# Kernel optimization log

Hardware: AMD Instinct MI355X
Metric: run time of the kernel (lower is better)

Reference implementation:

```python
import jax, jax.numpy as jnp
import numpy as np

L, H, NH, FF = 12, 768, 12, 3072
HD = H // NH
B, T = 8, 512
SCALE = 1.0 / float(np.sqrt(HD))
EPS = 1e-12


def setup_inputs() -> dict:
    key = jax.random.key(0)
    ks = jax.random.split(key, 10)
    s = jnp.float32(0.02)

    def p(k, shape):
        return jax.random.normal(k, shape, dtype=jnp.float32) * s

    return {
        "hidden_states": jax.random.normal(ks[0], (B, T, H), dtype=jnp.float32),
        "attention_mask": jnp.ones((B, T), dtype=jnp.float32),
        "Wq": p(ks[1], (L, H, H)), "bq": jnp.zeros((L, H), jnp.float32),
        "Wk": p(ks[2], (L, H, H)), "bk": jnp.zeros((L, H), jnp.float32),
        "Wv": p(ks[3], (L, H, H)), "bv": jnp.zeros((L, H), jnp.float32),
        "Wao": p(ks[4], (L, H, H)), "bao": jnp.zeros((L, H), jnp.float32),
        "ln1_g": jnp.ones((L, H), jnp.float32), "ln1_b": jnp.zeros((L, H), jnp.float32),
        "Wi": p(ks[5], (L, H, FF)), "bi": jnp.zeros((L, FF), jnp.float32),
        "Wo": p(ks[6], (L, FF, H)), "bo": jnp.zeros((L, H), jnp.float32),
        "ln2_g": jnp.ones((L, H), jnp.float32), "ln2_b": jnp.zeros((L, H), jnp.float32),
    }


def _layernorm(x, g, b):
    m = jnp.mean(x, axis=-1, keepdims=True)
    v = jnp.mean((x - m) ** 2, axis=-1, keepdims=True)
    return (x - m) * jax.lax.rsqrt(v + EPS) * g + b


def _encoder(hidden_states, attention_mask, params):
    # additive mask: (1 - mask) * -10000, broadcast to [B, 1, 1, T]
    add_mask = (1.0 - attention_mask)[:, None, None, :] * -10000.0

    def layer(x, p):
        wq, bq, wk, bk, wv, bv, wao, bao, g1, b1, wi, bi, wo, bo, g2, b2 = p
        q = (x @ wq + bq).reshape(B, T, NH, HD)
        k = (x @ wk + bk).reshape(B, T, NH, HD)
        v = (x @ wv + bv).reshape(B, T, NH, HD)
        scores = jnp.einsum('bihd,bjhd->bhij', q, k) * SCALE + add_mask
        probs = jax.nn.softmax(scores, axis=-1)  # dropout p=0 (eval)
        ctx = jnp.einsum('bhij,bjhd->bihd', probs, v).reshape(B, T, H)
        attn_out = _layernorm(ctx @ wao + bao + x, g1, b1)
        ff = jax.nn.gelu(attn_out @ wi + bi, approximate=False)
        out = _layernorm(ff @ wo + bo + attn_out, g2, b2)
        return out, None

    out, _ = jax.lax.scan(layer, hidden_states, params)
    return out


def reference(hidden_states, attention_mask, Wq, bq, Wk, bk, Wv, bv, Wao, bao,
              ln1_g, ln1_b, Wi, bi, Wo, bo, ln2_g, ln2_b):
    params = (Wq, bq, Wk, bk, Wv, bv, Wao, bao, ln1_g, ln1_b, Wi, bi, Wo, bo, ln2_g, ln2_b)
    return _encoder(hidden_states, attention_mask, params)
```

## Files before the change

### kernel.cpp

```cpp
#include <hip/hip_runtime.h>
#include <hip/hip_bf16.h>

typedef __bf16 bf16;
typedef __attribute__((ext_vector_type(8))) __bf16 bf16x8;
typedef __attribute__((ext_vector_type(4))) float f32x4;

#define MFMA16(a, b, c) __builtin_amdgcn_mfma_f32_16x16x32_bf16((a), (b), (c), 0, 0, 0)

#define SYNC_VM(N) do { asm volatile("s_waitcnt vmcnt(" #N ")" ::: "memory"); \
    __builtin_amdgcn_s_barrier(); __builtin_amdgcn_sched_barrier(0); } while (0)
#define SYNC_LGKM() do { asm volatile("s_waitcnt lgkmcnt(0)" ::: "memory"); \
    __builtin_amdgcn_s_barrier(); __builtin_amdgcn_sched_barrier(0); } while (0)

__device__ __forceinline__ void async16(const bf16* g, bf16* l) {
    __builtin_amdgcn_global_load_lds((__attribute__((address_space(1))) void*)(g),
                                     (__attribute__((address_space(3))) void*)(l), 16, 0, 0);
}

__device__ __forceinline__ void xcd_swizzle(int& bx, int& by, int& bz) {
    const int gx = gridDim.x, gy = gridDim.y;
    const int nwg = gx * gy * gridDim.z;
    const int lin = blockIdx.x + gx * (blockIdx.y + gy * blockIdx.z);
    const int xcd = lin & 7, seq = lin >> 3;
    const int q = nwg >> 3, r = nwg & 7;
    const int nl = (xcd < r ? xcd * (q + 1) : r * (q + 1) + (xcd - r) * q) + seq;
    bx = nl % gx;
    const int t = nl / gx;
    by = t % gy;
    bz = t / gy;
}

template <int MODE, int BM>
__global__ __launch_bounds__(256) void gemm_kernel(
    const bf16* __restrict__ A, const bf16* __restrict__ WT,
    const float* __restrict__ b0, const float* __restrict__ b1, const float* __restrict__ b2,
    int s1, int s2,
    void* __restrict__ o0, void* __restrict__ o1,
    int N, int K, int Kpart)
{
    constexpr int MT = BM / 32;
    __shared__ __align__(16) bf16 sA[2][BM * 32];
    __shared__ __align__(16) bf16 sB[2][128 * 32];

    const int tid  = threadIdx.x;
    const int lane = tid & 63;
    const int wave = tid >> 6;
    const int quad = lane >> 4;
    const int l15  = lane & 15;
    const int wm   = (wave >> 1) * (BM / 2);
    const int wn   = (wave & 1) * 64;

    int bxs, bys, bzs;
    xcd_swizzle(bxs, bys, bzs);
    const int bm = bys * BM;
    const int bn = bxs * 128;
    const int kbase = bzs * Kpart;

    f32x4 acc[MT][4];
#pragma unroll
    for (int i = 0; i < MT; i++)
#pragma unroll
        for (int j = 0; j < 4; j++)
#pragma unroll
            for (int r = 0; r < 4; r++) acc[i][j][r] = 0.0f;

    const int idx1 = tid + 256;
    const int ra0 = tid >> 2,  ca0 = (((tid  & 3) ^ ((ra0 >> 1) & 3)) * 8);
    const int rb1 = idx1 >> 2, cb1 = (((idx1 & 3) ^ ((rb1 >> 1) & 3)) * 8);

    const bf16* Arow0 = A + (size_t)(bm + ra0) * K + kbase + ca0;
    const bf16* Arow1 = (BM == 128) ? A + (size_t)(bm + rb1) * K + kbase + cb1 : A;
    const bf16* Brow0 = WT + (size_t)(bn + ra0) * K + kbase + ca0;
    const bf16* Brow1 = WT + (size_t)(bn + rb1) * K + kbase + cb1;

    const int nk = Kpart >> 5;

    async16(Arow0, sA[0] + tid * 8);
    if (BM == 128) async16(Arow1, sA[0] + idx1 * 8);
    async16(Brow0, sB[0] + tid * 8);
    async16(Brow1, sB[0] + idx1 * 8);

    const int chF = (quad ^ ((l15 >> 1) & 3)) * 8;

    int cur = 0;
    for (int kt = 0; kt < nk; kt++) {
        if (kt + 1 < nk) {
            const int ko = (kt + 1) * 32;
            async16(Arow0 + ko, sA[cur ^ 1] + tid * 8);
            if (BM == 128) async16(Arow1 + ko, sA[cur ^ 1] + idx1 * 8);
            async16(Brow0 + ko, sB[cur ^ 1] + tid * 8);
            async16(Brow1 + ko, sB[cur ^ 1] + idx1 * 8);
            if (BM == 128) SYNC_VM(4);
            else           SYNC_VM(3);
        } else {
            SYNC_VM(0);
        }
        bf16x8 af[MT], bfr[4];
#pragma unroll
        for (int i = 0; i < MT; i++)
            af[i] = *(const bf16x8*)(sA[cur] + (wm + i * 16 + l15) * 32 + chF);
#pragma unroll
        for (int i = 0; i < 4; i++)
            bfr[i] = *(const bf16x8*)(sB[cur] + (wn + i * 16 + l15) * 32 + chF);
#pragma unroll
        for (int mt = 0; mt < MT; mt++)
#pragma unroll
            for (int nt = 0; nt < 4; nt++)
                acc[mt][nt] = MFMA16(af[mt], bfr[nt], acc[mt][nt]);
        SYNC_LGKM();
        cur ^= 1;
    }

    void* outp = (bzs == 0) ? o0 : o1;

#pragma unroll
    for (int nt = 0; nt < 4; nt++) {
        const int col = bn + wn + nt * 16 + l15;
        float bias = 0.0f;
        if (MODE != 1)
            bias = (col < s1) ? b0[col] : (col < s2) ? b1[col - s1] : b2[col - s2];
#pragma unroll
        for (int mt = 0; mt < MT; mt++) {
#pragma unroll
            for (int r = 0; r < 4; r++) {
                const int row = bm + wm + mt * 16 + quad * 4 + r;
                float v = acc[mt][nt][r] + bias;
                if (MODE == 2) v = 0.5f * v * (1.0f + erff(v * 0.70710678118654752f));
                if (MODE == 1) ((float*)outp)[(size_t)row * N + col] = v;
                else           ((bf16*)outp)[(size_t)row * N + col] = (bf16)v;
            }
        }
    }
}

__global__ __launch_bounds__(256) void vtrans_kernel(
    const bf16* __restrict__ qkv, bf16* __restrict__ vT)
{
    const int bh = blockIdx.y;
    const int b = bh / 12, h = bh - b * 12;
    const int k0 = blockIdx.x * 128;
    __shared__ __align__(16) bf16 tile[128 * 72];
    const int tid = threadIdx.x;
    const bf16* src = qkv + (size_t)(b * 512 + k0) * 2304 + 1536 + h * 64;
#pragma unroll
    for (int i = 0; i < 4; i++) {
        const int idx = i * 256 + tid;
        const int r = idx >> 3, c = (idx & 7) * 8;
        *(uint4*)(tile + r * 72 + c) = *(const uint4*)(src + (size_t)r * 2304 + c);
    }
    __syncthreads();
    bf16* dst = vT + (size_t)bh * 64 * 512 + k0;
#pragma unroll
    for (int i = 0; i < 4; i++) {
        const int idx = i * 256 + tid;
        const int d = idx & 63, kg = idx >> 6;
        alignas(16) bf16 tmp[8];
#pragma unroll
        for (int e = 0; e < 8; e++) tmp[e] = tile[(kg * 8 + e) * 72 + d];
        *(uint4*)(dst + (size_t)d * 512 + kg * 8) = *(uint4*)tmp;
    }
}

__global__ __launch_bounds__(256) void attn_kernel(
    const bf16* __restrict__ qkv, const bf16* __restrict__ vT,
    const float* __restrict__ mask, bf16* __restrict__ ctx)
{
    int bxs, bys, bzs;
    xcd_swizzle(bxs, bys, bzs);
    const int b = bzs, h = bys, q0 = bxs * 32;
    const int bh = b * 12 + h;
    const int tid = threadIdx.x, lane = tid & 63, wave = tid >> 6;
    const int quad = lane >> 4, l15 = lane & 15;
    const int mt = wave & 1;
    const int whi = wave >> 1;

    __shared__ __align__(16) bf16 sKV[2][64 * 64];
    __shared__ __align__(16) bf16 sS[32 * 520];
    __shared__ float sAM[512];
    __shared__ float sRed[256];
    __shared__ float sRow[32];

    for (int i = tid; i < 512; i += 256)
        sAM[i] = (1.0f - mask[b * 512 + i]) * -10000.0f;

    const size_t RS = 2304;
    const bf16* Qrow = qkv + (size_t)(b * 512 + q0 + mt * 16 + l15) * RS + h * 64;
    const bf16x8 aQ0 = *(const bf16x8*)(Qrow + quad * 8);
    const bf16x8 aQ1 = *(const bf16x8*)(Qrow + 32 + quad * 8);

    const int c0 = tid, c1 = tid + 256;
    const int r0 = c0 >> 3, r1 = c1 >> 3;
    const int sc0 = ((c0 & 7) ^ (r0 & 7)) * 8;
    const int sc1 = ((c1 & 7) ^ (r1 & 7)) * 8;

    const bf16* Kbase = qkv + (size_t)(b * 512) * RS + 768 + h * 64;

    async16(Kbase + (size_t)(r0) * RS + sc0, (bf16*)sKV[0] + c0 * 8);
    async16(Kbase + (size_t)(r1) * RS + sc1, (bf16*)sKV[0] + c1 * 8);

#pragma unroll
    for (int kt = 0; kt < 8; kt++) {
        const int cur = kt & 1;
        if (kt < 7) {
            async16(Kbase + (size_t)((kt + 1) * 64 + r0) * RS + sc0, (bf16*)sKV[cur ^ 1] + c0 * 8);
            async16(Kbase + (size_t)((kt + 1) * 64 + r1) * RS + sc1, (bf16*)sKV[cur ^ 1] + c1 * 8);
            SYNC_VM(2);
        } else {
            SYNC_VM(0);
        }
#pragma unroll
        for (int n = 0; n < 2; n++) {
            const int nt = whi * 2 + n;
            const int krow = nt * 16 + l15;
            const int sw = krow & 7;
            bf16x8 bK0 = *(const bf16x8*)(sKV[cur] + krow * 64 + ((quad ^ sw) * 8));
            bf16x8 bK1 = *(const bf16x8*)(sKV[cur] + krow * 64 + (((4 + quad) ^ sw) * 8));
            f32x4 accS;
#pragma unroll
            for (int r = 0; r < 4; r++) accS[r] = 0.0f;
            accS = MFMA16(aQ0, bK0, accS);
            accS = MFMA16(aQ1, bK1, accS);
#pragma unroll
            for (int r = 0; r < 4; r++) {
                const int row = mt * 16 + quad * 4 + r;
                sS[row * 520 + kt * 64 + nt * 16 + l15] = (bf16)accS[r];
            }
        }
        SYNC_LGKM();
    }

    const bf16* Vbase = vT + (size_t)bh * 64 * 512;
    async16(Vbase + (size_t)r0 * 512 + sc0, (bf16*)sKV[0] + c0 * 8);
    async16(Vbase + (size_t)r1 * 512 + sc1, (bf16*)sKV[0] + c1 * 8);

    {
        const int r = tid >> 3, p = tid & 7;
        float mx = -1e30f;
#pragma unroll
        for (int t = 0; t < 8; t++) {
            const int v0 = (p + 8 * t) * 8;
            bf16x8 pv = *(const bf16x8*)(sS + r * 520 + v0);
#pragma unroll
            for (int e = 0; e < 8; e++)
                mx = fmaxf(mx, (float)pv[e] * 0.125f + sAM[v0 + e]);
        }
        sRed[r * 8 + p] = mx;
        SYNC_LGKM();
#pragma unroll
        for (int q = 0; q < 8; q++) mx = fmaxf(mx, sRed[r * 8 + q]);
        float sum = 0.0f;
#pragma unroll
        for (int t = 0; t < 8; t++) {
            const int v0 = (p + 8 * t) * 8;
            bf16x8 pv = *(const bf16x8*)(sS + r * 520 + v0);
            bf16x8 ev;
#pragma unroll
            for (int e = 0; e < 8; e++) {
                const float x = __expf((float)pv[e] * 0.125f + sAM[v0 + e] - mx);
                sum += x;
                ev[e] = (bf16)x;
            }
            *(bf16x8*)(sS + r * 520 + v0) = ev;
        }
        SYNC_LGKM();
        sRed[r * 8 + p] = sum;
        SYNC_LGKM();
        if (p == 0) {
            float s = 0.0f;
#pragma unroll
            for (int q = 0; q < 8; q++) s += sRed[r * 8 + q];
            sRow[r] = s;
        }
    }

    f32x4 accO[2];
#pragma unroll
    for (int i = 0; i < 2; i++)
#pragma unroll
        for (int r = 0; r < 4; r++) accO[i][r] = 0.0f;

#pragma unroll
    for (int kt = 0; kt < 8; kt++) {
        const int cur = kt & 1;
        if (kt < 7) {
            async16(Vbase + (size_t)r0 * 512 + (kt + 1) * 64 + sc0, (bf16*)sKV[cur ^ 1] + c0 * 8);
            async16(Vbase + (size_t)r1 * 512 + (kt + 1) * 64 + sc1, (bf16*)sKV[cur ^ 1] + c1 * 8);
            SYNC_VM(2);
        } else {
            SYNC_VM(0);
        }
#pragma unroll
        for (int kk = 0; kk < 2; kk++) {
            bf16x8 aP = *(const bf16x8*)(sS + (mt * 16 + l15) * 520 + kt * 64 + kk * 32 + quad * 8);
#pragma unroll
            for (int n = 0; n < 2; n++) {
                const int vrow = whi * 32 + n * 16 + l15;
                bf16x8 bV = *(const bf16x8*)(sKV[cur] + vrow * 64 + (((kk * 4 + quad) ^ (vrow & 7)) * 8));
                accO[n] = MFMA16(aP, bV, accO[n]);
            }
        }
        SYNC_LGKM();
    }
#pragma unroll
    for (int n = 0; n < 2; n++) {
#pragma unroll
        for (int r = 0; r < 4; r++) {
            const int row = mt * 16 + quad * 4 + r;
            const float o = accO[n][r] / sRow[row];
            ctx[(size_t)(b * 512 + q0 + row) * 768 + h * 64 + whi * 32 + n * 16 + l15] = (bf16)o;
        }
    }
}

template <int NP>
__global__ __launch_bounds__(256) void ln_kernel(
    const float* __restrict__ p0, const float* __restrict__ p1,
    const float* __restrict__ bias, const float* __restrict__ resid,
    const float* __restrict__ g, const float* __restrict__ bb,
    bf16* __restrict__ out_bf, float* __restrict__ out_f32)
{
    const int row = blockIdx.x;
    const int tid = threadIdx.x;
    __shared__ float sS[4], sQ[4];

    float x[3], s = 0.0f, sq = 0.0f;
#pragma unroll
    for (int j = 0; j < 3; j++) {
        const int c = tid + j * 256;
        const size_t idx = (size_t)row * 768 + c;
        float v = p0[idx] + bias[c] + resid[idx];
        if (NP > 1) v += p1[idx];
        x[j] = v; s += v; sq += v * v;
    }
#pragma unroll
    for (int off = 32; off; off >>= 1) { s += __shfl_down(s, off); sq += __shfl_down(sq, off); }
    if ((tid & 63) == 0) { sS[tid >> 6] = s; sQ[tid >> 6] = sq; }
    __syncthreads();
    s  = sS[0] + sS[1] + sS[2] + sS[3];
    sq = sQ[0] + sQ[1] + sQ[2] + sQ[3];
    const float mean = s * (1.0f / 768.0f);
    float var = sq * (1.0f / 768.0f) - mean * mean;
    var = fmaxf(var, 0.0f);
    const float rstd = rsqrtf(var + 1e-12f);
#pragma unroll
    for (int j = 0; j < 3; j++) {
        const int c = tid + j * 256;
        const float v = (x[j] - mean) * rstd * g[c] + bb[c];
        out_bf[(size_t)row * 768 + c] = (bf16)v;
        out_f32[(size_t)row * 768 + c] = v;
    }
}

__global__ __launch_bounds__(256) void transpose_kernel(
    const float* __restrict__ Wq, const float* __restrict__ Wk, const float* __restrict__ Wv,
    const float* __restrict__ Wao, const float* __restrict__ Wi, const float* __restrict__ Wo,
    bf16* __restrict__ wT)
{
    __shared__ bf16 tile[64 * 68];
    int id = blockIdx.x;
    const float* src; bf16* dst; int Kd, Nd;
    if (id < 576) {
        const int w = id / 144; id -= w * 144;
        Kd = 768; Nd = 768;
        src = (w == 0) ? Wq : (w == 1) ? Wk : (w == 2) ? Wv : Wao;
        dst = wT + (size_t)w * 589824;
    } else if (id < 1152) {
        id -= 576; Kd = 768; Nd = 3072; src = Wi; dst = wT + 2359296;
    } else {
        id -= 1152; Kd = 3072; Nd = 768; src = Wo; dst = wT + 4718592;
    }
    const int tn = Nd >> 6;
    const int tr = id / tn, tc = id - tr * tn;
    const int r0 = tr * 64, c0 = tc * 64;
    const int tid = threadIdx.x;

#pragma unroll
    for (int i = 0; i < 4; i++) {
        const int idx = i * 256 + tid;
        const int r = idx >> 4, c4 = (idx & 15) * 4;
        const float4 f = *(const float4*)(src + (size_t)(r0 + r) * Nd + c0 + c4);
        alignas(8) bf16 q[4] = {(bf16)f.x, (bf16)f.y, (bf16)f.z, (bf16)f.w};
        *(ushort4*)(tile + r * 68 + c4) = *(ushort4*)q;
    }
    __syncthreads();
#pragma unroll
    for (int i = 0; i < 4; i++) {
        const int idx = i * 256 + tid;
        const int n = idx >> 4, kc = (idx & 15) * 4;
        alignas(8) bf16 tmp[4];
#pragma unroll
        for (int e = 0; e < 4; e++) tmp[e] = tile[(kc + e) * 68 + n];
        *(ushort4*)(dst + (size_t)(c0 + n) * Kd + r0 + kc) = *(ushort4*)tmp;
    }
}

__global__ __launch_bounds__(256) void convert_kernel(
    const float* __restrict__ in, bf16* __restrict__ out, int n)
{
    const int i = blockIdx.x * 256 + threadIdx.x;
    if (i < n) out[i] = (bf16)in[i];
}

extern "C" void kernel_launch(void* const* d_in, const int* in_sizes, int n_in,
                              void* d_out, int out_size, void* d_ws, size_t ws_size,
                              hipStream_t stream)
{
    const float* hidden = (const float*)d_in[0];
    const float* mask   = (const float*)d_in[1];
    const float* Wq  = (const float*)d_in[2];  const float* bq  = (const float*)d_in[3];
    const float* Wk  = (const float*)d_in[4];  const float* bk  = (const float*)d_in[5];
    const float* Wv  = (const float*)d_in[6];  const float* bv  = (const float*)d_in[7];
    const float* Wao = (const float*)d_in[8];  const float* bao = (const float*)d_in[9];
    const float* g1  = (const float*)d_in[10]; const float* be1 = (const float*)d_in[11];
    const float* Wi  = (const float*)d_in[12]; const float* bi  = (const float*)d_in[13];
    const float* Wo  = (const float*)d_in[14]; const float* bo  = (const float*)d_in[15];
    const float* g2  = (const float*)d_in[16]; const float* be2 = (const float*)d_in[17];

    char* ws = (char*)d_ws;
    bf16*  wT    = (bf16*)(ws);
    bf16*  qkv   = (bf16*)(ws + 14155776);
    bf16*  vT    = (bf16*)(ws + 33030144);
    bf16*  ctx   = (bf16*)(ws + 39321600);
    bf16*  attnb = (bf16*)(ws + 45613056);
    bf16*  xb    = (bf16*)(ws + 51904512);
    float* xf    = (float*)(ws + 58195968);
    float* attnf = (float*)(ws + 70778880);
    bf16*  ffh   = (bf16*)(ws + 14155776);
    float* pA0   = (float*)(ws + 14155776);
    float* pF0   = (float*)(ws + 39321600);
    float* pF1   = (float*)(ws + 83361792);

    convert_kernel<<<12288, 256, 0, stream>>>(hidden, xb, 3145728);

    for (int l = 0; l < 12; l++) {
        transpose_kernel<<<1728, 256, 0, stream>>>(
            Wq + (size_t)l * 589824, Wk + (size_t)l * 589824, Wv + (size_t)l * 589824,
            Wao + (size_t)l * 589824, Wi + (size_t)l * 2359296, Wo + (size_t)l * 2359296, wT);

        gemm_kernel<0, 64><<<dim3(18, 64, 1), 256, 0, stream>>>(
            xb, wT, bq + l * 768, bk + l * 768, bv + l * 768, 768, 1536,
            qkv, nullptr, 2304, 768, 768);

        vtrans_kernel<<<dim3(4, 96), 256, 0, stream>>>(qkv, vT);

        attn_kernel<<<dim3(16, 12, 8), 256, 0, stream>>>(qkv, vT, mask, ctx);

        gemm_kernel<1, 64><<<dim3(6, 64, 1), 256, 0, stream>>>(
            ctx, wT + 1769472, nullptr, nullptr, nullptr, 0, 0,
            pA0, nullptr, 768, 768, 768);

        const float* resid1 = (l == 0) ? hidden : xf;
        ln_kernel<1><<<4096, 256, 0, stream>>>(
            pA0, nullptr, bao + l * 768, resid1, g1 + l * 768, be1 + l * 768, attnb, attnf);

        gemm_kernel<2, 128><<<dim3(24, 32, 1), 256, 0, stream>>>(
            attnb, wT + 2359296, bi + l * 3072, bi + l * 3072, bi + l * 3072, 3072, 3072,
            ffh, nullptr, 3072, 768, 768);

        gemm_kernel<1, 64><<<dim3(6, 64, 2), 256, 0, stream>>>(
            ffh, wT + 4718592, nullptr, nullptr, nullptr, 0, 0,
            pF0, pF1, 768, 3072, 1536);

        float* f32dst = (l == 11) ? (float*)d_out : xf;
        ln_kernel<2><<<4096, 256, 0, stream>>>(
            pF0, pF1, bo + l * 768, attnf, g2 + l * 768, be2 + l * 768, xb, f32dst);
    }
}
```

Before: 2.462 ms.

## Add single-wave 64x64 GEMM kernel and 3-way split-K for projections

```diff
diff --git a/kernel.cpp b/kernel.cpp
--- a/kernel.cpp
+++ b/kernel.cpp
@@ -28,6 +28,103 @@
     const int t = nl / gx;
     by = t % gy;
     bz = t / gy;
+}
+
+template <int MODE>
+__global__ __launch_bounds__(64) void gemm1w_kernel(
+    const bf16* __restrict__ A, const bf16* __restrict__ WT,
+    const float* __restrict__ b0, const float* __restrict__ b1, const float* __restrict__ b2,
+    int s1, int s2,
+    float* __restrict__ o0, float* __restrict__ o1, float* __restrict__ o2,
+    bf16* __restrict__ ob,
+    int N, int K, int Kpart)
+{
+    __shared__ __align__(16) bf16 sA[2][64 * 32];
+    __shared__ __align__(16) bf16 sB[2][64 * 32];
+
+    const int l    = threadIdx.x;
+    const int quad = l >> 4;
+    const int l15  = l & 15;
+
+    int bxs, bys, bzs;
+    xcd_swizzle(bxs, bys, bzs);
+    const int bm = bys * 64;
+    const int bn = bxs * 64;
+    const int kbase = bzs * Kpart;
+
+    int rS[4], cS[4];
+#pragma unroll
+    for (int g = 0; g < 4; g++) {
+        rS[g] = g * 16 + (l >> 2);
+        cS[g] = (((l & 3) ^ ((rS[g] >> 1) & 3)) * 8);
+    }
+    const bf16* Abase = A  + kbase;
+    const bf16* Bbase = WT + kbase;
+
+    const int nk = Kpart >> 5;
+
+    auto stage = [&](int kt, int buf) {
+#pragma unroll
+        for (int g = 0; g < 4; g++)
+            async16(Abase + (size_t)(bm + rS[g]) * K + kt * 32 + cS[g], sA[buf] + (g * 64 + l) * 8);
+#pragma unroll
+        for (int g = 0; g < 4; g++)
+            async16(Bbase + (size_t)(bn + rS[g]) * K + kt * 32 + cS[g], sB[buf] + (g * 64 + l) * 8);
+    };
+
+    f32x4 acc[4][4];
+#pragma unroll
+    for (int i = 0; i < 4; i++)
+#pragma unroll
+        for (int j = 0; j < 4; j++)
+#pragma unroll
+            for (int r = 0; r < 4; r++) acc[i][j][r] = 0.0f;
+
+    stage(0, 0);
+    if (nk > 1) stage(1, 1);
+
+    const int chF = (quad ^ ((l15 >> 1) & 3)) * 8;
+
+    for (int kt = 0; kt < nk; kt++) {
+        const int cur = kt & 1;
+        if (kt + 1 < nk) { asm volatile("s_waitcnt vmcnt(8)" ::: "memory"); }
+        else             { asm volatile("s_waitcnt vmcnt(0)" ::: "memory"); }
+        __builtin_amdgcn_sched_barrier(0);
+        bf16x8 af[4], bfr[4];
+#pragma unroll
+        for (int i = 0; i < 4; i++)
+            af[i] = *(const bf16x8*)(sA[cur] + (i * 16 + l15) * 32 + chF);
+#pragma unroll
+        for (int i = 0; i < 4; i++)
+            bfr[i] = *(const bf16x8*)(sB[cur] + (i * 16 + l15) * 32 + chF);
+#pragma unroll
+        for (int mt = 0; mt < 4; mt++)
+#pragma unroll
+            for (int nt = 0; nt < 4; nt++)
+                acc[mt][nt] = MFMA16(af[mt], bfr[nt], acc[mt][nt]);
+        __builtin_amdgcn_sched_barrier(0);
+        if (kt + 2 < nk) stage(kt + 2, cur);
+    }
+
+    float* po = (bzs == 0) ? o0 : (bzs == 1) ? o1 : o2;
+
+#pragma unroll
+    for (int nt = 0; nt < 4; nt++) {
+        const int col = bn + nt * 16 + l15;
+        float bias = 0.0f;
+        if (MODE == 0)
+            bias = (col < s1) ? b0[col] : (col < s2) ? b1[col - s1] : b2[col - s2];
+#pragma unroll
+        for (int mt = 0; mt < 4; mt++) {
+#pragma unroll
+            for (int r = 0; r < 4; r++) {
+                const int row = bm + mt * 16 + quad * 4 + r;
+                const float v = acc[mt][nt][r] + bias;
+                if (MODE == 1) po[(size_t)row * N + col] = v;
+                else           ob[(size_t)row * N + col] = (bf16)v;
+            }
+        }
+    }
 }
 
 template <int MODE, int BM>
@@ -314,10 +411,10 @@
 
 template <int NP>
 __global__ __launch_bounds__(256) void ln_kernel(
-    const float* __restrict__ p0, const float* __restrict__ p1,
-    const float* __restrict__ bias, const float* __restrict__ resid,
-    const float* __restrict__ g, const float* __restrict__ bb,
-    bf16* __restrict__ out_bf, float* __restrict__ out_f32)
+    const float* p0, const float* p1, const float* p2,
+    const float* bias, const float* resid,
+    const float* g, const float* bb,
+    bf16* out_bf, float* out_f32)
 {
     const int row = blockIdx.x;
     const int tid = threadIdx.x;
@@ -330,6 +427,7 @@
         const size_t idx = (size_t)row * 768 + c;
         float v = p0[idx] + bias[c] + resid[idx];
         if (NP > 1) v += p1[idx];
+        if (NP > 2) v += p2[idx];
         x[j] = v; s += v; sq += v * v;
     }
 #pragma unroll
@@ -427,8 +525,11 @@
     float* attnf = (float*)(ws + 70778880);
     bf16*  ffh   = (bf16*)(ws + 14155776);
     float* pA0   = (float*)(ws + 14155776);
+    float* pA1   = (float*)(ws + 26738688);
+    float* pA2   = (float*)(ws + 83361792);
     float* pF0   = (float*)(ws + 39321600);
-    float* pF1   = (float*)(ws + 83361792);
+    float* pF1   = (float*)(ws + 58195968);
+    float* pF2   = (float*)(ws + 83361792);
 
     convert_kernel<<<12288, 256, 0, stream>>>(hidden, xb, 3145728);
 
@@ -437,32 +538,32 @@
             Wq + (size_t)l * 589824, Wk + (size_t)l * 589824, Wv + (size_t)l * 589824,
             Wao + (size_t)l * 589824, Wi + (size_t)l * 2359296, Wo + (size_t)l * 2359296, wT);
 
-        gemm_kernel<0, 64><<<dim3(18, 64, 1), 256, 0, stream>>>(
+        gemm1w_kernel<0><<<dim3(36, 64, 1), 64, 0, stream>>>(
             xb, wT, bq + l * 768, bk + l * 768, bv + l * 768, 768, 1536,
-            qkv, nullptr, 2304, 768, 768);
+            nullptr, nullptr, nullptr, qkv, 2304, 768, 768);
 
         vtrans_kernel<<<dim3(4, 96), 256, 0, stream>>>(qkv, vT);
 
         attn_kernel<<<dim3(16, 12, 8), 256, 0, stream>>>(qkv, vT, mask, ctx);
 
-        gemm_kernel<1, 64><<<dim3(6, 64, 1), 256, 0, stream>>>(
+        gemm1w_kernel<1><<<dim3(12, 64, 3), 64, 0, stream>>>(
             ctx, wT + 1769472, nullptr, nullptr, nullptr, 0, 0,
-            pA0, nullptr, 768, 768, 768);
+            pA0, pA1, pA2, nullptr, 768, 768, 256);
 
         const float* resid1 = (l == 0) ? hidden : xf;
-        ln_kernel<1><<<4096, 256, 0, stream>>>(
-            pA0, nullptr, bao + l * 768, resid1, g1 + l * 768, be1 + l * 768, attnb, attnf);
+        ln_kernel<3><<<4096, 256, 0, stream>>>(
+            pA0, pA1, pA2, bao + l * 768, resid1, g1 + l * 768, be1 + l * 768, attnb, attnf);
 
         gemm_kernel<2, 128><<<dim3(24, 32, 1), 256, 0, stream>>>(
             attnb, wT + 2359296, bi + l * 3072, bi + l * 3072, bi + l * 3072, 3072, 3072,
             ffh, nullptr, 3072, 768, 768);
 
-        gemm_kernel<1, 64><<<dim3(6, 64, 2), 256, 0, stream>>>(
+        gemm1w_kernel<1><<<dim3(12, 64, 3), 64, 0, stream>>>(
             ffh, wT + 4718592, nullptr, nullptr, nullptr, 0, 0,
-            pF0, pF1, 768, 3072, 1536);
+            pF0, pF1, pF2, nullptr, 768, 3072, 1024);
 
         float* f32dst = (l == 11) ? (float*)d_out : xf;
-        ln_kernel<2><<<4096, 256, 0, stream>>>(
-            pF0, pF1, bo + l * 768, attnf, g2 + l * 768, be2 + l * 768, xb, f32dst);
-    }
-}
+        ln_kernel<3><<<4096, 256, 0, stream>>>(
+            pF0, pF1, pF2, bo + l * 768, attnf, g2 + l * 768, be2 + l * 768, xb, f32dst);
+    }
+}
```

Result: slower. 2.799 ms (+13.7%).

## Triple-buffer GEMM K-loop and split-K the attention output projection

Applied to the files above, without the earlier changes.

```diff
diff --git a/kernel.cpp b/kernel.cpp
--- a/kernel.cpp
+++ b/kernel.cpp
@@ -7,10 +7,10 @@
 
 #define MFMA16(a, b, c) __builtin_amdgcn_mfma_f32_16x16x32_bf16((a), (b), (c), 0, 0, 0)
 
-#define SYNC_VM(N) do { asm volatile("s_waitcnt vmcnt(" #N ")" ::: "memory"); \
-    __builtin_amdgcn_s_barrier(); __builtin_amdgcn_sched_barrier(0); } while (0)
-#define SYNC_LGKM() do { asm volatile("s_waitcnt lgkmcnt(0)" ::: "memory"); \
-    __builtin_amdgcn_s_barrier(); __builtin_amdgcn_sched_barrier(0); } while (0)
+#define WAIT_VM(N) asm volatile("s_waitcnt vmcnt(" #N ")" ::: "memory")
+#define BAR() do { __builtin_amdgcn_s_barrier(); __builtin_amdgcn_sched_barrier(0); } while (0)
+#define SYNC_VM(N) do { WAIT_VM(N); BAR(); } while (0)
+#define SYNC_LGKM() do { asm volatile("s_waitcnt lgkmcnt(0)" ::: "memory"); BAR(); } while (0)
 
 __device__ __forceinline__ void async16(const bf16* g, bf16* l) {
     __builtin_amdgcn_global_load_lds((__attribute__((address_space(1))) void*)(g),
@@ -39,8 +39,8 @@
     int N, int K, int Kpart)
 {
     constexpr int MT = BM / 32;
-    __shared__ __align__(16) bf16 sA[2][BM * 32];
-    __shared__ __align__(16) bf16 sB[2][128 * 32];
+    __shared__ __align__(16) bf16 sA[3][BM * 32];
+    __shared__ __align__(16) bf16 sB[3][128 * 32];
 
     const int tid  = threadIdx.x;
     const int lane = tid & 63;
@@ -75,26 +75,31 @@
 
     const int nk = Kpart >> 5;
 
-    async16(Arow0, sA[0] + tid * 8);
-    if (BM == 128) async16(Arow1, sA[0] + idx1 * 8);
-    async16(Brow0, sB[0] + tid * 8);
-    async16(Brow1, sB[0] + idx1 * 8);
+    auto stage = [&](int kt, int buf) {
+        const int ko = kt * 32;
+        async16(Arow0 + ko, sA[buf] + tid * 8);
+        if (BM == 128) async16(Arow1 + ko, sA[buf] + idx1 * 8);
+        async16(Brow0 + ko, sB[buf] + tid * 8);
+        async16(Brow1 + ko, sB[buf] + idx1 * 8);
+    };
+
+    stage(0, 0);
+    if (nk > 1) stage(1, 1);
+    if (nk > 2) stage(2, 2);
 
     const int chF = (quad ^ ((l15 >> 1) & 3)) * 8;
 
     int cur = 0;
     for (int kt = 0; kt < nk; kt++) {
-        if (kt + 1 < nk) {
-            const int ko = (kt + 1) * 32;
-            async16(Arow0 + ko, sA[cur ^ 1] + tid * 8);
-            if (BM == 128) async16(Arow1 + ko, sA[cur ^ 1] + idx1 * 8);
-            async16(Brow0 + ko, sB[cur ^ 1] + tid * 8);
-            async16(Brow1 + ko, sB[cur ^ 1] + idx1 * 8);
-            if (BM == 128) SYNC_VM(4);
-            else           SYNC_VM(3);
+        if (kt + 2 < nk) {
+            if (BM == 128) { WAIT_VM(8); } else { WAIT_VM(6); }
+        } else if (kt + 1 < nk) {
+            if (BM == 128) { WAIT_VM(4); } else { WAIT_VM(3); }
         } else {
-            SYNC_VM(0);
-        }
+            WAIT_VM(0);
+        }
+        BAR();
+
         bf16x8 af[MT], bfr[4];
 #pragma unroll
         for (int i = 0; i < MT; i++)
@@ -107,8 +112,10 @@
 #pragma unroll
             for (int nt = 0; nt < 4; nt++)
                 acc[mt][nt] = MFMA16(af[mt], bfr[nt], acc[mt][nt]);
-        SYNC_LGKM();
-        cur ^= 1;
+
+        SYNC_LGKM();
+        if (kt + 3 < nk) stage(kt + 3, cur);
+        cur = (cur == 2) ? 0 : cur + 1;
     }
 
     void* outp = (bzs == 0) ? o0 : o1;
@@ -427,6 +434,7 @@
     float* attnf = (float*)(ws + 70778880);
     bf16*  ffh   = (bf16*)(ws + 14155776);
     float* pA0   = (float*)(ws + 14155776);
+    float* pA1   = (float*)(ws + 26738688);
     float* pF0   = (float*)(ws + 39321600);
     float* pF1   = (float*)(ws + 83361792);
 
@@ -445,13 +453,13 @@
 
         attn_kernel<<<dim3(16, 12, 8), 256, 0, stream>>>(qkv, vT, mask, ctx);
 
-        gemm_kernel<1, 64><<<dim3(6, 64, 1), 256, 0, stream>>>(
+        gemm_kernel<1, 64><<<dim3(6, 64, 2), 256, 0, stream>>>(
             ctx, wT + 1769472, nullptr, nullptr, nullptr, 0, 0,
-            pA0, nullptr, 768, 768, 768);
+            pA0, pA1, 768, 768, 384);
 
         const float* resid1 = (l == 0) ? hidden : xf;
-        ln_kernel<1><<<4096, 256, 0, stream>>>(
-            pA0, nullptr, bao + l * 768, resid1, g1 + l * 768, be1 + l * 768, attnb, attnf);
+        ln_kernel<2><<<4096, 256, 0, stream>>>(
+            pA0, pA1, bao + l * 768, resid1, g1 + l * 768, be1 + l * 768, attnb, attnf);
 
         gemm_kernel<2, 128><<<dim3(24, 32, 1), 256, 0, stream>>>(
             attnb, wT + 2359296, bi + l * 3072, bi + l * 3072, bi + l * 3072, 3072, 3072,
```

New measurement: 2.550 ms. +3.6%, slower.

## Fuse V-transpose into QKV GEMM and overlap next-layer weight prep with FFN kernels

Applied to the files above, without the earlier changes.

```diff
diff --git a/kernel.cpp b/kernel.cpp
--- a/kernel.cpp
+++ b/kernel.cpp
@@ -7,17 +7,27 @@
 
 #define MFMA16(a, b, c) __builtin_amdgcn_mfma_f32_16x16x32_bf16((a), (b), (c), 0, 0, 0)
 
-#define SYNC_VM(N) do { asm volatile("s_waitcnt vmcnt(" #N ")" ::: "memory"); \
-    __builtin_amdgcn_s_barrier(); __builtin_amdgcn_sched_barrier(0); } while (0)
-#define SYNC_LGKM() do { asm volatile("s_waitcnt lgkmcnt(0)" ::: "memory"); \
-    __builtin_amdgcn_s_barrier(); __builtin_amdgcn_sched_barrier(0); } while (0)
+#define WAIT_VM(N) asm volatile("s_waitcnt vmcnt(" #N ")" ::: "memory")
+#define BAR() do { __builtin_amdgcn_s_barrier(); __builtin_amdgcn_sched_barrier(0); } while (0)
+#define SYNC_VM(N) do { WAIT_VM(N); BAR(); } while (0)
+#define SYNC_LGKM() do { asm volatile("s_waitcnt lgkmcnt(0)" ::: "memory"); BAR(); } while (0)
 
 __device__ __forceinline__ void async16(const bf16* g, bf16* l) {
     __builtin_amdgcn_global_load_lds((__attribute__((address_space(1))) void*)(g),
                                      (__attribute__((address_space(3))) void*)(l), 16, 0, 0);
 }
 
-__device__ __forceinline__ void xcd_swizzle(int& bx, int& by, int& bz) {
+__device__ __forceinline__ void xcd_swizzle2(int& bx, int& by) {
+    const int gx = gridDim.x, gy = gridDim.y;
+    const int nwg = gx * gy;
+    const int lin = blockIdx.x + gx * blockIdx.y;
+    const int xcd = lin & 7, seq = lin >> 3;
+    const int q = nwg >> 3, r = nwg & 7;
+    const int nl = (xcd < r ? xcd * (q + 1) : r * (q + 1) + (xcd - r) * q) + seq;
+    bx = nl % gx;
+    by = nl / gx;
+}
+__device__ __forceinline__ void xcd_swizzle3(int& bx, int& by, int& bz) {
     const int gx = gridDim.x, gy = gridDim.y;
     const int nwg = gx * gy * gridDim.z;
     const int lin = blockIdx.x + gx * (blockIdx.y + gy * blockIdx.z);
@@ -30,19 +40,74 @@
     bz = t / gy;
 }
 
-template <int MODE, int BM>
+__device__ __forceinline__ void xpose_tile(
+    int id, const float* Wq, const float* Wk, const float* Wv, const float* Wao,
+    const float* Wi, const float* Wo, bf16* wT, bf16* tile, int tid)
+{
+    const float* src; bf16* dst; int Nd;
+    if (id < 576) {
+        const int w = id / 144; id -= w * 144;
+        Nd = 768;
+        src = (w == 0) ? Wq : (w == 1) ? Wk : (w == 2) ? Wv : Wao;
+        dst = wT + (size_t)w * 589824;
+    } else if (id < 1152) {
+        id -= 576; Nd = 3072; src = Wi; dst = wT + 2359296;
+    } else {
+        id -= 1152; Nd = 768; src = Wo; dst = wT + 4718592;
+    }
+    const int Kd = (Nd == 3072) ? 768 : ((src == Wo) ? 3072 : 768);
+    const int tn = Nd >> 6;
+    const int tr = id / tn, tc = id - tr * tn;
+    const int r0 = tr * 64, c0 = tc * 64;
+
+#pragma unroll
+    for (int i = 0; i < 4; i++) {
+        const int idx = i * 256 + tid;
+        const int r = idx >> 4, c4 = (idx & 15) * 4;
+        const float4 f = *(const float4*)(src + (size_t)(r0 + r) * Nd + c0 + c4);
+        alignas(8) bf16 q[4] = {(bf16)f.x, (bf16)f.y, (bf16)f.z, (bf16)f.w};
+        *(ushort4*)(tile + r * 68 + c4) = *(ushort4*)q;
+    }
+    __syncthreads();
+#pragma unroll
+    for (int i = 0; i < 4; i++) {
+        const int idx = i * 256 + tid;
+        const int n = idx >> 4, kc = (idx & 15) * 4;
+        alignas(8) bf16 tmp[4];
+#pragma unroll
+        for (int e = 0; e < 4; e++) tmp[e] = tile[(kc + e) * 68 + n];
+        *(ushort4*)(dst + (size_t)(c0 + n) * Kd + r0 + kc) = *(ushort4*)tmp;
+    }
+}
+
+template <int MODE, int BM, int PACK>
 __global__ __launch_bounds__(256) void gemm_kernel(
     const bf16* __restrict__ A, const bf16* __restrict__ WT,
     const float* __restrict__ b0, const float* __restrict__ b1, const float* __restrict__ b2,
     int s1, int s2,
-    void* __restrict__ o0, void* __restrict__ o1,
+    void* __restrict__ o0, void* __restrict__ o1, bf16* __restrict__ vTout,
+    const float* __restrict__ xWq, const float* __restrict__ xWk,
+    const float* __restrict__ xWv, const float* __restrict__ xWao,
+    bf16* __restrict__ wTnext,
     int N, int K, int Kpart)
 {
     constexpr int MT = BM / 32;
-    __shared__ __align__(16) bf16 sA[2][BM * 32];
-    __shared__ __align__(16) bf16 sB[2][128 * 32];
-
-    const int tid  = threadIdx.x;
+    constexpr int SBYTES = (2 * (BM * 32) + 2 * (128 * 32)) * 2;
+    __shared__ __align__(16) char smem[SBYTES];
+    bf16* sA = (bf16*)smem;
+    bf16* sB = (bf16*)(smem + 2 * BM * 32 * 2);
+
+    const int tid = threadIdx.x;
+
+    if (PACK && blockIdx.z == 1) {
+        const int flat = blockIdx.y * gridDim.x + blockIdx.x;
+        if (flat < 576 && wTnext)
+            xpose_tile(flat, xWq, xWk, xWv, xWao, nullptr, nullptr, wTnext,
+                       (bf16*)smem, tid);
+        return;
+    }
+    const int kslice = PACK ? 0 : blockIdx.z;
+
     const int lane = tid & 63;
     const int wave = tid >> 6;
     const int quad = lane >> 4;
@@ -50,11 +115,11 @@
     const int wm   = (wave >> 1) * (BM / 2);
     const int wn   = (wave & 1) * 64;
 
-    int bxs, bys, bzs;
-    xcd_swizzle(bxs, bys, bzs);
+    int bxs, bys;
+    xcd_swizzle2(bxs, bys);
     const int bm = bys * BM;
     const int bn = bxs * 128;
-    const int kbase = bzs * Kpart;
+    const int kbase = kslice * Kpart;
 
     f32x4 acc[MT][4];
 #pragma unroll
@@ -75,10 +140,10 @@
 
     const int nk = Kpart >> 5;
 
-    async16(Arow0, sA[0] + tid * 8);
-    if (BM == 128) async16(Arow1, sA[0] + idx1 * 8);
-    async16(Brow0, sB[0] + tid * 8);
-    async16(Brow1, sB[0] + idx1 * 8);
+    async16(Arow0, sA + tid * 8);
+    if (BM == 128) async16(Arow1, sA + idx1 * 8);
+    async16(Brow0, sB + tid * 8);
+    async16(Brow1, sB + idx1 * 8);
 
     const int chF = (quad ^ ((l15 >> 1) & 3)) * 8;
 
@@ -86,22 +151,25 @@
     for (int kt = 0; kt < nk; kt++) {
         if (kt + 1 < nk) {
             const int ko = (kt + 1) * 32;
-            async16(Arow0 + ko, sA[cur ^ 1] + tid * 8);
-            if (BM == 128) async16(Arow1 + ko, sA[cur ^ 1] + idx1 * 8);
-            async16(Brow0 + ko, sB[cur ^ 1] + tid * 8);
-            async16(Brow1 + ko, sB[cur ^ 1] + idx1 * 8);
+            const int nb = (cur ^ 1);
+            async16(Arow0 + ko, sA + nb * BM * 32 + tid * 8);
+            if (BM == 128) async16(Arow1 + ko, sA + nb * BM * 32 + idx1 * 8);
+            async16(Brow0 + ko, sB + nb * 128 * 32 + tid * 8);
+            async16(Brow1 + ko, sB + nb * 128 * 32 + idx1 * 8);
             if (BM == 128) SYNC_VM(4);
             else           SYNC_VM(3);
         } else {
             SYNC_VM(0);
         }
+        const bf16* sAc = sA + cur * BM * 32;
+        const bf16* sBc = sB + cur * 128 * 32;
         bf16x8 af[MT], bfr[4];
 #pragma unroll
         for (int i = 0; i < MT; i++)
-            af[i] = *(const bf16x8*)(sA[cur] + (wm + i * 16 + l15) * 32 + chF);
+            af[i] = *(const bf16x8*)(sAc + (wm + i * 16 + l15) * 32 + chF);
 #pragma unroll
         for (int i = 0; i < 4; i++)
-            bfr[i] = *(const bf16x8*)(sB[cur] + (wn + i * 16 + l15) * 32 + chF);
+            bfr[i] = *(const bf16x8*)(sBc + (wn + i * 16 + l15) * 32 + chF);
 #pragma unroll
         for (int mt = 0; mt < MT; mt++)
 #pragma unroll
@@ -111,7 +179,7 @@
         cur ^= 1;
     }
 
-    void* outp = (bzs == 0) ? o0 : o1;
+    void* outp = (kslice == 0) ? o0 : o1;
 
 #pragma unroll
     for (int nt = 0; nt < 4; nt++) {
@@ -119,54 +187,41 @@
         float bias = 0.0f;
         if (MODE != 1)
             bias = (col < s1) ? b0[col] : (col < s2) ? b1[col - s1] : b2[col - s2];
-#pragma unroll
-        for (int mt = 0; mt < MT; mt++) {
-#pragma unroll
-            for (int r = 0; r < 4; r++) {
-                const int row = bm + wm + mt * 16 + quad * 4 + r;
-                float v = acc[mt][nt][r] + bias;
-                if (MODE == 2) v = 0.5f * v * (1.0f + erff(v * 0.70710678118654752f));
-                if (MODE == 1) ((float*)outp)[(size_t)row * N + col] = v;
-                else           ((bf16*)outp)[(size_t)row * N + col] = (bf16)v;
+        if (MODE == 0 && col >= s2) {
+            const int hd = col - s2, h = hd >> 6, d = hd & 63;
+#pragma unroll
+            for (int mt = 0; mt < MT; mt++) {
+                const int row0 = bm + wm + mt * 16 + quad * 4;
+                const int b = row0 >> 9, key = row0 & 511;
+                alignas(8) bf16 tmp[4];
+#pragma unroll
+                for (int r = 0; r < 4; r++) tmp[r] = (bf16)(acc[mt][nt][r] + bias);
+                *(ushort4*)(vTout + (((size_t)(b * 12 + h)) << 15) + (d << 9) + key)
+                    = *(ushort4*)tmp;
             }
-        }
-    }
-}
-
-__global__ __launch_bounds__(256) void vtrans_kernel(
-    const bf16* __restrict__ qkv, bf16* __restrict__ vT)
-{
-    const int bh = blockIdx.y;
-    const int b = bh / 12, h = bh - b * 12;
-    const int k0 = blockIdx.x * 128;
-    __shared__ __align__(16) bf16 tile[128 * 72];
-    const int tid = threadIdx.x;
-    const bf16* src = qkv + (size_t)(b * 512 + k0) * 2304 + 1536 + h * 64;
-#pragma unroll
-    for (int i = 0; i < 4; i++) {
-        const int idx = i * 256 + tid;
-        const int r = idx >> 3, c = (idx & 7) * 8;
-        *(uint4*)(tile + r * 72 + c) = *(const uint4*)(src + (size_t)r * 2304 + c);
-    }
-    __syncthreads();
-    bf16* dst = vT + (size_t)bh * 64 * 512 + k0;
-#pragma unroll
-    for (int i = 0; i < 4; i++) {
-        const int idx = i * 256 + tid;
-        const int d = idx & 63, kg = idx >> 6;
-        alignas(16) bf16 tmp[8];
-#pragma unroll
-        for (int e = 0; e < 8; e++) tmp[e] = tile[(kg * 8 + e) * 72 + d];
-        *(uint4*)(dst + (size_t)d * 512 + kg * 8) = *(uint4*)tmp;
+        } else {
+#pragma unroll
+            for (int mt = 0; mt < MT; mt++) {
+#pragma unroll
+                for (int r = 0; r < 4; r++) {
+                    const int row = bm + wm + mt * 16 + quad * 4 + r;
+                    float v = acc[mt][nt][r] + bias;
+                    if (MODE == 2) v = 0.5f * v * (1.0f + erff(v * 0.70710678118654752f));
+                    if (MODE == 1)      ((float*)outp)[(size_t)row * N + col] = v;
+                    else if (MODE == 0) ((bf16*)outp)[(size_t)row * s2 + col] = (bf16)v;
+                    else                ((bf16*)outp)[(size_t)row * N + col] = (bf16)v;
+                }
+            }
+        }
     }
 }
 
 __global__ __launch_bounds__(256) void attn_kernel(
-    const bf16* __restrict__ qkv, const bf16* __restrict__ vT,
+    const bf16* __restrict__ qk, const bf16* __restrict__ vT,
     const float* __restrict__ mask, bf16* __restrict__ ctx)
 {
     int bxs, bys, bzs;
-    xcd_swizzle(bxs, bys, bzs);
+    xcd_swizzle3(bxs, bys, bzs);
     const int b = bzs, h = bys, q0 = bxs * 32;
     const int bh = b * 12 + h;
     const int tid = threadIdx.x, lane = tid & 63, wave = tid >> 6;
@@ -183,8 +238,8 @@
     for (int i = tid; i < 512; i += 256)
         sAM[i] = (1.0f - mask[b * 512 + i]) * -10000.0f;
 
-    const size_t RS = 2304;
-    const bf16* Qrow = qkv + (size_t)(b * 512 + q0 + mt * 16 + l15) * RS + h * 64;
+    const size_t RS = 1536;
+    const bf16* Qrow = qk + (size_t)(b * 512 + q0 + mt * 16 + l15) * RS + h * 64;
     const bf16x8 aQ0 = *(const bf16x8*)(Qrow + quad * 8);
     const bf16x8 aQ1 = *(const bf16x8*)(Qrow + 32 + quad * 8);
 
@@ -193,7 +248,7 @@
     const int sc0 = ((c0 & 7) ^ (r0 & 7)) * 8;
     const int sc1 = ((c1 & 7) ^ (r1 & 7)) * 8;
 
-    const bf16* Kbase = qkv + (size_t)(b * 512) * RS + 768 + h * 64;
+    const bf16* Kbase = qk + (size_t)(b * 512) * RS + 768 + h * 64;
 
     async16(Kbase + (size_t)(r0) * RS + sc0, (bf16*)sKV[0] + c0 * 8);
     async16(Kbase + (size_t)(r1) * RS + sc1, (bf16*)sKV[0] + c1 * 8);
@@ -312,13 +367,23 @@
     }
 }
 
-template <int NP>
+template <int NP, int PACK>
 __global__ __launch_bounds__(256) void ln_kernel(
-    const float* __restrict__ p0, const float* __restrict__ p1,
-    const float* __restrict__ bias, const float* __restrict__ resid,
-    const float* __restrict__ g, const float* __restrict__ bb,
-    bf16* __restrict__ out_bf, float* __restrict__ out_f32)
+    const float* p0, const float* p1,
+    const float* bias, const float* resid,
+    const float* g, const float* bb,
+    bf16* out_bf, float* out_f32,
+    const float* xWi, const float* xWo, bf16* wTnext)
 {
+    if constexpr (PACK) {
+        __shared__ __align__(16) bf16 xtile[64 * 68];
+        if (blockIdx.x >= 4096) {
+            if (wTnext)
+                xpose_tile(576 + (blockIdx.x - 4096), nullptr, nullptr, nullptr,
+                           nullptr, xWi, xWo, wTnext, xtile, threadIdx.x);
+            return;
+        }
+    }
     const int row = blockIdx.x;
     const int tid = threadIdx.x;
     __shared__ float sS[4], sQ[4];
@@ -351,54 +416,20 @@
     }
 }
 
-__global__ __launch_bounds__(256) void transpose_kernel(
-    const float* __restrict__ Wq, const float* __restrict__ Wk, const float* __restrict__ Wv,
-    const float* __restrict__ Wao, const float* __restrict__ Wi, const float* __restrict__ Wo,
+__global__ __launch_bounds__(256) void prep_kernel(
+    const float* __restrict__ hidden, bf16* __restrict__ xb,
+    const float* __restrict__ Wq, const float* __restrict__ Wk,
+    const float* __restrict__ Wv, const float* __restrict__ Wao,
+    const float* __restrict__ Wi, const float* __restrict__ Wo,
     bf16* __restrict__ wT)
 {
-    __shared__ bf16 tile[64 * 68];
-    int id = blockIdx.x;
-    const float* src; bf16* dst; int Kd, Nd;
-    if (id < 576) {
-        const int w = id / 144; id -= w * 144;
-        Kd = 768; Nd = 768;
-        src = (w == 0) ? Wq : (w == 1) ? Wk : (w == 2) ? Wv : Wao;
-        dst = wT + (size_t)w * 589824;
-    } else if (id < 1152) {
-        id -= 576; Kd = 768; Nd = 3072; src = Wi; dst = wT + 2359296;
-    } else {
-        id -= 1152; Kd = 3072; Nd = 768; src = Wo; dst = wT + 4718592;
-    }
-    const int tn = Nd >> 6;
-    const int tr = id / tn, tc = id - tr * tn;
-    const int r0 = tr * 64, c0 = tc * 64;
-    const int tid = threadIdx.x;
-
-#pragma unroll
-    for (int i = 0; i < 4; i++) {
-        const int idx = i * 256 + tid;
-        const int r = idx >> 4, c4 = (idx & 15) * 4;
-        const float4 f = *(const float4*)(src + (size_t)(r0 + r) * Nd + c0 + c4);
-        alignas(8) bf16 q[4] = {(bf16)f.x, (bf16)f.y, (bf16)f.z, (bf16)f.w};
-        *(ushort4*)(tile + r * 68 + c4) = *(ushort4*)q;
-    }
-    __syncthreads();
-#pragma unroll
-    for (int i = 0; i < 4; i++) {
-        const int idx = i * 256 + tid;
-        const int n = idx >> 4, kc = (idx & 15) * 4;
-        alignas(8) bf16 tmp[4];
-#pragma unroll
-        for (int e = 0; e < 4; e++) tmp[e] = tile[(kc + e) * 68 + n];
-        *(ushort4*)(dst + (size_t)(c0 + n) * Kd + r0 + kc) = *(ushort4*)tmp;
-    }
-}
-
-__global__ __launch_bounds__(256) void convert_kernel(
-    const float* __restrict__ in, bf16* __restrict__ out, int n)
-{
-    const int i = blockIdx.x * 256 + threadIdx.x;
-    if (i < n) out[i] = (bf16)in[i];
+    __shared__ __align__(16) bf16 tile[64 * 68];
+    if (blockIdx.x < 12288) {
+        const int i = blockIdx.x * 256 + threadIdx.x;
+        if (i < 3145728) xb[i] = (bf16)hidden[i];
+        return;
+    }
+    xpose_tile(blockIdx.x - 12288, Wq, Wk, Wv, Wao, Wi, Wo, wT, tile, threadIdx.x);
 }
 
 extern "C" void kernel_launch(void* const* d_in, const int* in_sizes, int n_in,
@@ -418,51 +449,58 @@
 
     char* ws = (char*)d_ws;
     bf16*  wT    = (bf16*)(ws);
-    bf16*  qkv   = (bf16*)(ws + 14155776);
-    bf16*  vT    = (bf16*)(ws + 33030144);
-    bf16*  ctx   = (bf16*)(ws + 39321600);
-    bf16*  attnb = (bf16*)(ws + 45613056);
-    bf16*  xb    = (bf16*)(ws + 51904512);
-    float* xf    = (float*)(ws + 58195968);
-    float* attnf = (float*)(ws + 70778880);
+    bf16*  qk    = (bf16*)(ws + 14155776);
+    bf16*  vT    = (bf16*)(ws + 26738688);
+    bf16*  ctx   = (bf16*)(ws + 33030144);
+    bf16*  attnb = (bf16*)(ws + 39321600);
+    bf16*  xb    = (bf16*)(ws + 45613056);
+    float* xf    = (float*)(ws + 51904512);
+    float* attnf = (float*)(ws + 64487424);
     bf16*  ffh   = (bf16*)(ws + 14155776);
     float* pA0   = (float*)(ws + 14155776);
-    float* pF0   = (float*)(ws + 39321600);
-    float* pF1   = (float*)(ws + 83361792);
-
-    convert_kernel<<<12288, 256, 0, stream>>>(hidden, xb, 3145728);
+    float* pA1   = (float*)(ws + 77070336);
+    float* pF0   = (float*)(ws + 77070336);
+    float* pF1   = (float*)(ws + 51904512);
+
+    prep_kernel<<<14016, 256, 0, stream>>>(hidden, xb, Wq, Wk, Wv, Wao, Wi, Wo, wT);
 
     for (int l = 0; l < 12; l++) {
-        transpose_kernel<<<1728, 256, 0, stream>>>(
-            Wq + (size_t)l * 589824, Wk + (size_t)l * 589824, Wv + (size_t)l * 589824,
-            Wao + (size_t)l * 589824, Wi + (size_t)l * 2359296, Wo + (size_t)l * 2359296, wT);
-
-        gemm_kernel<0, 64><<<dim3(18, 64, 1), 256, 0, stream>>>(
+        const int ln = l + 1;
+        bf16* wTn = (l < 11) ? wT : nullptr;
+
+        gemm_kernel<0, 64, 0><<<dim3(18, 64, 1), 256, 0, stream>>>(
             xb, wT, bq + l * 768, bk + l * 768, bv + l * 768, 768, 1536,
-            qkv, nullptr, 2304, 768, 768);
-
-        vtrans_kernel<<<dim3(4, 96), 256, 0, stream>>>(qkv, vT);
-
-        attn_kernel<<<dim3(16, 12, 8), 256, 0, stream>>>(qkv, vT, mask, ctx);
-
-        gemm_kernel<1, 64><<<dim3(6, 64, 1), 256, 0, stream>>>(
+            qk, nullptr, vT, nullptr, nullptr, nullptr, nullptr, nullptr,
+            2304, 768, 768);
+
+        attn_kernel<<<dim3(16, 12, 8), 256, 0, stream>>>(qk, vT, mask, ctx);
+
+        gemm_kernel<1, 64, 0><<<dim3(6, 64, 2), 256, 0, stream>>>(
             ctx, wT + 1769472, nullptr, nullptr, nullptr, 0, 0,
-            pA0, nullptr, 768, 768, 768);
+            pA0, pA1, nullptr, nullptr, nullptr, nullptr, nullptr, nullptr,
+            768, 768, 384);
 
         const float* resid1 = (l == 0) ? hidden : xf;
-        ln_kernel<1><<<4096, 256, 0, stream>>>(
-            pA0, nullptr, bao + l * 768, resid1, g1 + l * 768, be1 + l * 768, attnb, attnf);
-
-        gemm_kernel<2, 128><<<dim3(24, 32, 1), 256, 0, stream>>>(
+        ln_kernel<2, 0><<<4096, 256, 0, stream>>>(
+            pA0, pA1, bao + l * 768, resid1, g1 + l * 768, be1 + l * 768,
+            attnb, attnf, nullptr, nullptr, nullptr);
+
+        gemm_kernel<2, 128, 1><<<dim3(24, 32, 2), 256, 0, stream>>>(
             attnb, wT + 2359296, bi + l * 3072, bi + l * 3072, bi + l * 3072, 3072, 3072,
-            ffh, nullptr, 3072, 768, 768);
-
-        gemm_kernel<1, 64><<<dim3(6, 64, 2), 256, 0, stream>>>(
+            ffh, nullptr, nullptr,
+            Wq + (size_t)(ln % 12) * 589824, Wk + (size_t)(ln % 12) * 589824,
+            Wv + (size_t)(ln % 12) * 589824, Wao + (size_t)(ln % 12) * 589824, wTn,
+            3072, 768, 768);
+
+        gemm_kernel<1, 64, 0><<<dim3(6, 64, 2), 256, 0, stream>>>(
             ffh, wT + 4718592, nullptr, nullptr, nullptr, 0, 0,
-            pF0, pF1, 768, 3072, 1536);
+            pF0, pF1, nullptr, nullptr, nullptr, nullptr, nullptr, nullptr,
+            768, 3072, 1536);
 
         float* f32dst = (l == 11) ? (float*)d_out : xf;
-        ln_kernel<2><<<4096, 256, 0, stream>>>(
-            pF0, pF1, bo + l * 768, attnf, g2 + l * 768, be2 + l * 768, xb, f32dst);
-    }
-}
+        ln_kernel<2, 1><<<4096 + 1152, 256, 0, stream>>>(
+            pF0, pF1, bo + l * 768, attnf, g2 + l * 768, be2 + l * 768,
+            xb, f32dst,
+            Wi + (size_t)(ln % 12) * 2359296, Wo + (size_t)(ln % 12) * 2359296, wTn);
+    }
+}
```

Measured after the change: 2.361 ms. 1.04x faster.
